# Kernel optimization log

Hardware: AMD Instinct MI355X
Metric: run time of the kernel (lower is better)

The kernel has to match this reference:

```python
import jax, jax.numpy as jnp
import numpy as np

B, D, L, H = 256, 256, 256, 512  # batch, driving series (input_size), (T-1)*features_num, hidden_size


def setup_inputs() -> dict:
    key = jax.random.key(0)
    ks = jax.random.split(key, 6)
    s = 1.0 / np.sqrt(H).astype(np.float32)
    return {
        "input_data": jax.random.normal(ks[0], (B, D, L), jnp.float32),
        # attn_linear: Linear(2H + L -> 1)
        "W_attn": jax.random.normal(ks[1], (2 * H + L, 1), jnp.float32) * 0.02,
        "b_attn": jnp.zeros((1,), jnp.float32),
        # single-layer LSTM params, torch gate order (i, f, g, o)
        "W_ih": jax.random.uniform(ks[2], (4 * H, D), jnp.float32, -s, s),
        "W_hh": jax.random.uniform(ks[3], (4 * H, H), jnp.float32, -s, s),
        "b_ih": jax.random.uniform(ks[4], (4 * H,), jnp.float32, -s, s),
        "b_hh": jnp.zeros((4 * H,), jnp.float32),
    }


def reference(input_data, W_attn, b_attn, W_ih, W_hh, b_ih, b_hh):
    Bn, Dn, Ln = input_data.shape
    Hn = W_hh.shape[1]
    # Split attn weight instead of materializing concat([h, c, x]) each step:
    # score = [h | c | x_hist] @ W_attn + b == h@Wh + c@Wc + x_hist@Wx + b
    Wh = W_attn[:Hn, 0]
    Wc = W_attn[Hn:2 * Hn, 0]
    Wx = W_attn[2 * Hn:, 0]
    # x-history contribution is constant across steps -> hoist out of the scan
    x_proj = jnp.einsum("bdl,l->bd", input_data, Wx) + b_attn[0]  # [B, D]
    bias = b_ih + b_hh
    xs = jnp.moveaxis(input_data, 2, 0)  # [L, B, D] per-step columns x_t

    def step(carry, xt):
        h, c = carry  # [B, H] each
        score = x_proj + (h @ Wh + c @ Wc)[:, None]  # [B, D]
        attn = jax.nn.softmax(score, axis=1)  # softmax over driving series
        w = attn * xt  # attention-weighted input, [B, D]
        gates = w @ W_ih.T + h @ W_hh.T + bias  # [B, 4H]
        i, f, g, o = jnp.split(gates, 4, axis=1)
        c2 = jax.nn.sigmoid(f) * c + jax.nn.sigmoid(i) * jnp.tanh(g)
        h2 = jax.nn.sigmoid(o) * jnp.tanh(c2)
        return (h2, c2), (w, h2)

    h0 = jnp.zeros((Bn, Hn), input_data.dtype)
    c0 = jnp.zeros((Bn, Hn), input_data.dtype)
    _, (ws, hs) = jax.lax.scan(step, (h0, c0), xs)
    # match torch's final permute: [total_x_features, B, *] -> [B, total_x_features, *]
    return jnp.moveaxis(ws, 0, 1), jnp.moveaxis(hs, 0, 1)
```

## Files before the change

### kernel.cpp

```cpp
#include <hip/hip_runtime.h>
#include <hip/hip_fp16.h>

typedef _Float16 half8 __attribute__((ext_vector_type(8)));
typedef float floatx4 __attribute__((ext_vector_type(4)));
typedef int intx4 __attribute__((ext_vector_type(4)));

#define NB 256
#define ND 256
#define NL 256
#define NH 512

__global__ void k_xproj(const float* __restrict__ x, const float* __restrict__ Wattn,
                        float* __restrict__ xproj) {
    __shared__ float wx[NL];
    const int tid = threadIdx.x;
    wx[tid] = Wattn[2 * NH + tid];
    __syncthreads();
    const int wid = tid >> 6, lane = tid & 63;
    const int row = blockIdx.x * 4 + wid;
    const float4 v = ((const float4*)(x + (size_t)row * NL))[lane];
    float s = v.x * wx[lane * 4] + v.y * wx[lane * 4 + 1] +
              v.z * wx[lane * 4 + 2] + v.w * wx[lane * 4 + 3];
    #pragma unroll
    for (int off = 32; off; off >>= 1) s += __shfl_down(s, off);
    if (lane == 0) xproj[row] = s;
}

__global__ void k_softmax(const float* __restrict__ xproj, float* __restrict__ attn) {
    const int b = blockIdx.x, tid = threadIdx.x;
    __shared__ float red[8];
    float v = xproj[b * ND + tid];
    float m = v;
    #pragma unroll
    for (int off = 32; off; off >>= 1) m = fmaxf(m, __shfl_down(m, off));
    const int wid = tid >> 6, lane = tid & 63;
    if (lane == 0) red[wid] = m;
    __syncthreads();
    if (tid == 0) {
        float mm = fmaxf(fmaxf(red[0], red[1]), fmaxf(red[2], red[3]));
        red[4] = mm;
    }
    __syncthreads();
    const float e = expf(v - red[4]);
    float s = e;
    #pragma unroll
    for (int off = 32; off; off >>= 1) s += __shfl_down(s, off);
    if (lane == 0) red[wid] = s;
    __syncthreads();
    if (tid == 0) red[5] = red[0] + red[1] + red[2] + red[3];
    __syncthreads();
    attn[b * ND + tid] = e / red[5];
}

__global__ void k_trans(const float* __restrict__ x, const float* __restrict__ attn,
                        float* __restrict__ ws_out, _Float16* __restrict__ w16) {
    __shared__ float tile[64][65];
    const int bid = blockIdx.x;
    const int b = bid >> 4, ti = (bid >> 2) & 3, tj = bid & 3;
    const int tx = threadIdx.x & 63, ty = threadIdx.x >> 6;
    const int d0 = ti * 64, l0 = tj * 64;
    const float* xb = x + ((size_t)b * ND + d0) * NL + l0;
    #pragma unroll
    for (int r = ty; r < 64; r += 4) tile[r][tx] = xb[(size_t)r * NL + tx];
    __syncthreads();
    const float af = attn[b * ND + d0 + tx];
    #pragma unroll
    for (int r = ty; r < 64; r += 4) {
        const int tt = l0 + r;
        const float val = af * tile[tx][r];
        ws_out[((size_t)b * NL + tt) * ND + d0 + tx] = val;
        w16[((size_t)tt * NB + b) * ND + d0 + tx] = (_Float16)val;
    }
}

__global__ void k_wsplit(const float* __restrict__ Whh, const float* __restrict__ Wih,
                         _Float16* __restrict__ hi, _Float16* __restrict__ lo,
                         _Float16* __restrict__ wih16) {
    const int idx = blockIdx.x * 256 + threadIdx.x;
    const float w = Whh[idx];
    const _Float16 h = (_Float16)w;
    hi[idx] = h;
    lo[idx] = (_Float16)(w - (float)h);
    if (idx < 4 * NH * ND) wih16[idx] = (_Float16)Wih[idx];
}

__launch_bounds__(512, 2)
__global__ void k_recur(const _Float16* __restrict__ whhHi, const _Float16* __restrict__ whhLo,
                        const _Float16* __restrict__ wih16, const _Float16* __restrict__ w16,
                        const float* __restrict__ b_ih, const float* __restrict__ b_hh,
                        _Float16* __restrict__ h16,
                        int* __restrict__ flags,
                        float* __restrict__ out_hs)
{
    __shared__ char smem[40960];
    const int tid = threadIdx.x;
    const int wid = tid >> 6, lane = tid & 63;
    const int bid = blockIdx.x;
    const int m = bid & 15, hb = bid >> 4;
    const int b0 = m * 16;
    const int gate = wid >> 1, half = wid & 1;
    const int jb = gate * 512 + hb * 32 + half * 16;

    half8 bhhH[16], bhhL[16], bihF[8];
    const int bcol = jb + (lane & 15);
    const int krow = (lane >> 4) * 8;
    #pragma unroll
    for (int kk = 0; kk < 16; ++kk) {
        bhhH[kk] = *(const half8*)(whhHi + (size_t)bcol * NH + kk * 32 + krow);
        bhhL[kk] = *(const half8*)(whhLo + (size_t)bcol * NH + kk * 32 + krow);
    }
    #pragma unroll
    for (int kk = 0; kk < 8; ++kk)
        bihF[kk] = *(const half8*)(wih16 + (size_t)bcol * ND + kk * 32 + krow);

    const int bl = tid >> 5, hl = tid & 31;
    float bias_[4];
    #pragma unroll
    for (int g = 0; g < 4; ++g) {
        const int j = g * 512 + hb * 32 + hl;
        bias_[g] = b_ih[j] + b_hh[j];
    }
    float c = 0.f;
    float* hsOut = out_hs + (size_t)(b0 + bl) * NL * NH + hb * 32 + hl;
    _Float16* hWr = h16 + (size_t)(b0 + bl) * NH + hb * 32 + hl;

    const int arow = lane & 15;
    const int aq = (lane >> 4) * 16;
    const int aswz = (arow & 7) << 4;

    {
        const char* wsrc = (const char*)(w16 + (size_t)b0 * ND);
        const intx4 wd = *(const intx4*)(wsrc + tid * 16);
        const int wr = tid >> 5;
        *(intx4*)(smem + 16384 + ((tid * 16) ^ ((wr & 7) << 4))) = wd;
    }
    __syncthreads();

    #pragma unroll 1
    for (int t = 0; t < NL; ++t) {
        const int cur = t & 1, nxt = (t + 1) & 1;

        const int tp = (t + 1 < NL) ? t + 1 : t;
        const intx4 wpref = *(const intx4*)(
            (const char*)(w16 + ((size_t)tp * NB + b0) * ND) + tid * 16);

        floatx4 accC = {0.f, 0.f, 0.f, 0.f};
        #pragma unroll
        for (int kk = 0; kk < 8; ++kk) {
            const int waddr = 16384 + 8192 * cur + ((((arow << 9) + (kk << 6) + aq)) ^ aswz);
            const half8 a = *(const half8*)(smem + waddr);
            accC = __builtin_amdgcn_mfma_f32_16x16x32_f16(a, bihF[kk], accC, 0, 0, 0);
        }

        if (t > 0 && wid == 0) {
            const int* fp = flags + (m << 4) + (lane & 15);
            int v;
            do {
                asm volatile(
                    "global_load_dword %0, %1, off sc0 sc1\n\t"
                    "s_waitcnt vmcnt(0)"
                    : "=v"(v) : "v"(fp) : "memory");
            } while (!__all(v >= t));
        }
        __syncthreads();

        {
            const char* hsrc = (const char*)(h16 + (size_t)cur * NB * NH + (size_t)b0 * NH);
            intx4 d0, d1;
            asm volatile(
                "global_load_dwordx4 %0, %2, off sc0 sc1\n\t"
                "global_load_dwordx4 %1, %3, off sc0 sc1\n\t"
                "s_waitcnt vmcnt(0)"
                : "=v"(d0), "=v"(d1)
                : "v"(hsrc + tid * 16), "v"(hsrc + tid * 16 + 8192) : "memory");
            const int r0 = tid >> 6;
            const int r1 = (tid + 512) >> 6;
            *(intx4*)(smem + ((tid * 16) ^ ((r0 & 7) << 4))) = d0;
            *(intx4*)(smem + ((tid * 16 + 8192) ^ ((r1 & 7) << 4))) = d1;
            const int wr = tid >> 5;
            *(intx4*)(smem + 16384 + 8192 * nxt + ((tid * 16) ^ ((wr & 7) << 4))) = wpref;
        }
        __syncthreads();

        floatx4 accA = {0.f, 0.f, 0.f, 0.f};
        floatx4 accB = {0.f, 0.f, 0.f, 0.f};
        #pragma unroll
        for (int kk = 0; kk < 16; ++kk) {
            const int aaddr = ((arow << 10) + (kk << 6) + aq) ^ aswz;
            const half8 a = *(const half8*)(smem + aaddr);
            accA = __builtin_amdgcn_mfma_f32_16x16x32_f16(a, bhhH[kk], accA, 0, 0, 0);
            accB = __builtin_amdgcn_mfma_f32_16x16x32_f16(a, bhhL[kk], accB, 0, 0, 0);
        }
        const floatx4 f = (accA + accB) + accC;

        {
            float* accL = (float*)(smem + 32768);
            const int colw = lane & 15, rowq = (lane >> 4) * 4;
            #pragma unroll
            for (int r = 0; r < 4; ++r)
                accL[wid * 256 + (rowq + r) * 16 + colw] = f[r];
        }
        __syncthreads();

        float h2;
        {
            const float* accL = (const float*)(smem + 32768);
            const int hq = hl >> 4, cidx = hl & 15;
            const int off = bl * 16 + cidx;
            const float pi = accL[(0 + hq) * 256 + off] + bias_[0];
            const float pf = accL[(2 + hq) * 256 + off] + bias_[1];
            const float pg = accL[(4 + hq) * 256 + off] + bias_[2];
            const float po = accL[(6 + hq) * 256 + off] + bias_[3];
            const float si = 1.f / (1.f + __expf(-pi));
            const float sf = 1.f / (1.f + __expf(-pf));
            const float so = 1.f / (1.f + __expf(-po));
            float e2 = __expf(-2.f * fabsf(pg));
            float tg = (1.f - e2) / (1.f + e2);
            tg = (pg < 0.f) ? -tg : tg;
            c = sf * c + si * tg;
            float e2c = __expf(-2.f * fabsf(c));
            float tc = (1.f - e2c) / (1.f + e2c);
            tc = (c < 0.f) ? -tc : tc;
            h2 = so * tc;
            const _Float16 hh = (_Float16)h2;
            const unsigned int hv = (unsigned int)__builtin_bit_cast(unsigned short, hh);
            const void* hp = hWr + (size_t)nxt * NB * NH;
            asm volatile("global_store_short %0, %1, off sc0 sc1"
                         :: "v"(hp), "v"(hv) : "memory");
        }

        if (t < NL - 1) {
            asm volatile("s_waitcnt vmcnt(0)" ::: "memory");
            __syncthreads();
            if (tid == 0) {
                const int* tp2 = flags + (m << 4) + hb;
                const int tv = t + 1;
                asm volatile("global_store_dword %0, %1, off sc0 sc1"
                             :: "v"(tp2), "v"(tv) : "memory");
            }
        }
        hsOut[(size_t)t * NH] = h2;
    }
}

extern "C" void kernel_launch(void* const* d_in, const int* in_sizes, int n_in,
                              void* d_out, int out_size, void* d_ws, size_t ws_size,
                              hipStream_t stream) {
    const float* x     = (const float*)d_in[0];
    const float* Wattn = (const float*)d_in[1];
    const float* Wih   = (const float*)d_in[3];
    const float* Whh   = (const float*)d_in[4];
    const float* bih   = (const float*)d_in[5];
    const float* bhh   = (const float*)d_in[6];

    float* ws_out = (float*)d_out;
    float* hs_out = ws_out + (size_t)NB * NL * ND;

    char* ws = (char*)d_ws;
    int*      flags = (int*)(ws + 0);
    float*    attn  = (float*)(ws + 4096);
    float*    xproj = (float*)(ws + 4096 + 262144);
    _Float16* h16   = (_Float16*)(ws + 1048576);
    _Float16* whhHi = (_Float16*)(ws + 2097152);
    _Float16* whhLo = (_Float16*)(ws + 2097152 + 2097152);
    _Float16* wih16 = (_Float16*)(ws + 6291456);
    _Float16* w16   = (_Float16*)(ws + 8388608);

    hipMemsetAsync(flags, 0, 4096, stream);
    hipMemsetAsync(h16, 0, (size_t)NB * NH * sizeof(_Float16), stream);

    k_xproj  <<<16384, 256, 0, stream>>>(x, Wattn, xproj);
    k_softmax<<<256,   256, 0, stream>>>(xproj, attn);
    k_trans  <<<4096,  256, 0, stream>>>(x, attn, ws_out, w16);
    k_wsplit <<<4096,  256, 0, stream>>>(Whh, Wih, whhHi, whhLo, wih16);
    k_recur  <<<256,   512, 0, stream>>>(whhHi, whhLo, wih16, w16, bih, bhh,
                                         h16, flags, hs_out);
}
```

Baseline: 721.8 us.

## Replace flag-based inter-block sync with step-tagged hidden-state words

The recurrent kernel no longer publishes a per-block progress flag after a barrier and vmcnt drain. Instead, each fp16 hidden value is stored as a 32-bit word whose upper 16 bits carry the step number. Consumer threads spin directly on the h data until every tag matches the expected step, then unpack the values into shared memory. This takes the flag store, the flag poll, one block-wide barrier and both memsets off the per-step critical path. In exchange it doubles the hidden-state global traffic and relies on stale tags from earlier launches never matching the expected step.

```diff
diff --git a/kernel.cpp b/kernel.cpp
--- a/kernel.cpp
+++ b/kernel.cpp
@@ -88,8 +88,7 @@
 __global__ void k_recur(const _Float16* __restrict__ whhHi, const _Float16* __restrict__ whhLo,
                         const _Float16* __restrict__ wih16, const _Float16* __restrict__ w16,
                         const float* __restrict__ b_ih, const float* __restrict__ b_hh,
-                        _Float16* __restrict__ h16,
-                        int* __restrict__ flags,
+                        unsigned int* __restrict__ h32,
                         float* __restrict__ out_hs)
 {
     __shared__ char smem[40960];
@@ -122,11 +121,16 @@
     }
     float c = 0.f;
     float* hsOut = out_hs + (size_t)(b0 + bl) * NL * NH + hb * 32 + hl;
-    _Float16* hWr = h16 + (size_t)(b0 + bl) * NH + hb * 32 + hl;
+    unsigned int* hWr = h32 + (size_t)(b0 + bl) * NH + hb * 32 + hl;
 
     const int arow = lane & 15;
     const int aq = (lane >> 4) * 16;
     const int aswz = (arow & 7) << 4;
+
+    const int hrow = tid >> 5;
+    const int hcol16 = (tid & 31) * 16;
+    const int hbase = (hrow << 10) + (tid & 31) * 32;
+    const int hswz = (hrow & 7) << 4;
 
     {
         const char* wsrc = (const char*)(w16 + (size_t)b0 * ND);
@@ -152,31 +156,47 @@
             accC = __builtin_amdgcn_mfma_f32_16x16x32_f16(a, bihF[kk], accC, 0, 0, 0);
         }
 
-        if (t > 0 && wid == 0) {
-            const int* fp = flags + (m << 4) + (lane & 15);
-            int v;
-            do {
+        if (t > 0) {
+            const unsigned int* hsrc =
+                h32 + (size_t)cur * NB * NH + (size_t)(b0 + hrow) * NH + hcol16;
+            intx4 q0, q1, q2, q3;
+            const unsigned int et = (unsigned int)t;
+            while (true) {
                 asm volatile(
-                    "global_load_dword %0, %1, off sc0 sc1\n\t"
+                    "global_load_dwordx4 %0, %4, off sc0 sc1\n\t"
+                    "global_load_dwordx4 %1, %4, off offset:16 sc0 sc1\n\t"
+                    "global_load_dwordx4 %2, %4, off offset:32 sc0 sc1\n\t"
+                    "global_load_dwordx4 %3, %4, off offset:48 sc0 sc1\n\t"
                     "s_waitcnt vmcnt(0)"
-                    : "=v"(v) : "v"(fp) : "memory");
-            } while (!__all(v >= t));
-        }
-        __syncthreads();
-
+                    : "=v"(q0), "=v"(q1), "=v"(q2), "=v"(q3)
+                    : "v"(hsrc) : "memory");
+                bool ok = true;
+                #pragma unroll
+                for (int i = 0; i < 4; ++i) {
+                    ok &= (((unsigned int)q0[i]) >> 16) == et;
+                    ok &= (((unsigned int)q1[i]) >> 16) == et;
+                    ok &= (((unsigned int)q2[i]) >> 16) == et;
+                    ok &= (((unsigned int)q3[i]) >> 16) == et;
+                }
+                if (ok) break;
+            }
+            intx4 d0, d1;
+            d0[0] = (q0[0] & 0xffff) | (q0[1] << 16);
+            d0[1] = (q0[2] & 0xffff) | (q0[3] << 16);
+            d0[2] = (q1[0] & 0xffff) | (q1[1] << 16);
+            d0[3] = (q1[2] & 0xffff) | (q1[3] << 16);
+            d1[0] = (q2[0] & 0xffff) | (q2[1] << 16);
+            d1[1] = (q2[2] & 0xffff) | (q2[3] << 16);
+            d1[2] = (q3[0] & 0xffff) | (q3[1] << 16);
+            d1[3] = (q3[2] & 0xffff) | (q3[3] << 16);
+            *(intx4*)(smem + (hbase ^ hswz)) = d0;
+            *(intx4*)(smem + ((hbase + 16) ^ hswz)) = d1;
+        } else {
+            const intx4 z = {0, 0, 0, 0};
+            *(intx4*)(smem + (hbase ^ hswz)) = z;
+            *(intx4*)(smem + ((hbase + 16) ^ hswz)) = z;
+        }
         {
-            const char* hsrc = (const char*)(h16 + (size_t)cur * NB * NH + (size_t)b0 * NH);
-            intx4 d0, d1;
-            asm volatile(
-                "global_load_dwordx4 %0, %2, off sc0 sc1\n\t"
-                "global_load_dwordx4 %1, %3, off sc0 sc1\n\t"
-                "s_waitcnt vmcnt(0)"
-                : "=v"(d0), "=v"(d1)
-                : "v"(hsrc + tid * 16), "v"(hsrc + tid * 16 + 8192) : "memory");
-            const int r0 = tid >> 6;
-            const int r1 = (tid + 512) >> 6;
-            *(intx4*)(smem + ((tid * 16) ^ ((r0 & 7) << 4))) = d0;
-            *(intx4*)(smem + ((tid * 16 + 8192) ^ ((r1 & 7) << 4))) = d1;
             const int wr = tid >> 5;
             *(intx4*)(smem + 16384 + 8192 * nxt + ((tid * 16) ^ ((wr & 7) << 4))) = wpref;
         }
@@ -223,21 +243,12 @@
             tc = (c < 0.f) ? -tc : tc;
             h2 = so * tc;
             const _Float16 hh = (_Float16)h2;
-            const unsigned int hv = (unsigned int)__builtin_bit_cast(unsigned short, hh);
+            const unsigned int hv =
+                ((unsigned int)(t + 1) << 16) |
+                (unsigned int)__builtin_bit_cast(unsigned short, hh);
             const void* hp = hWr + (size_t)nxt * NB * NH;
-            asm volatile("global_store_short %0, %1, off sc0 sc1"
+            asm volatile("global_store_dword %0, %1, off sc0 sc1"
                          :: "v"(hp), "v"(hv) : "memory");
-        }
-
-        if (t < NL - 1) {
-            asm volatile("s_waitcnt vmcnt(0)" ::: "memory");
-            __syncthreads();
-            if (tid == 0) {
-                const int* tp2 = flags + (m << 4) + hb;
-                const int tv = t + 1;
-                asm volatile("global_store_dword %0, %1, off sc0 sc1"
-                             :: "v"(tp2), "v"(tv) : "memory");
-            }
         }
         hsOut[(size_t)t * NH] = h2;
     }
@@ -257,22 +268,18 @@
     float* hs_out = ws_out + (size_t)NB * NL * ND;
 
     char* ws = (char*)d_ws;
-    int*      flags = (int*)(ws + 0);
     float*    attn  = (float*)(ws + 4096);
     float*    xproj = (float*)(ws + 4096 + 262144);
-    _Float16* h16   = (_Float16*)(ws + 1048576);
+    unsigned int* h32 = (unsigned int*)(ws + 1048576);
     _Float16* whhHi = (_Float16*)(ws + 2097152);
     _Float16* whhLo = (_Float16*)(ws + 2097152 + 2097152);
     _Float16* wih16 = (_Float16*)(ws + 6291456);
     _Float16* w16   = (_Float16*)(ws + 8388608);
-
-    hipMemsetAsync(flags, 0, 4096, stream);
-    hipMemsetAsync(h16, 0, (size_t)NB * NH * sizeof(_Float16), stream);
 
     k_xproj  <<<16384, 256, 0, stream>>>(x, Wattn, xproj);
     k_softmax<<<256,   256, 0, stream>>>(xproj, attn);
     k_trans  <<<4096,  256, 0, stream>>>(x, attn, ws_out, w16);
     k_wsplit <<<4096,  256, 0, stream>>>(Whh, Wih, whhHi, whhLo, wih16);
     k_recur  <<<256,   512, 0, stream>>>(whhHi, whhLo, wih16, w16, bih, bhh,
-                                         h16, flags, hs_out);
-}
+                                         h32, hs_out);
+}
```

Result: faster. 695.8 us (-3.6%).
